# Kernel tuning notes

Measured on AMD Instinct MI355X. Metric: run time of the kernel, lower is better.

Reference implementation:

```python
import jax, jax.numpy as jnp
import numpy as np

WIN = 11  # hard-coded window size in the original module

def sinusoidal_pe(L, D):
    pos = jnp.arange(L, dtype=jnp.float32)[:, None]
    div = jnp.exp(jnp.arange(0, D, 2, dtype=jnp.float32) * (-np.log(10000.0) / D))
    pe = jnp.zeros((L, D), dtype=jnp.float32)
    pe = pe.at[:, 0::2].set(jnp.sin(pos * div))
    pe = pe.at[:, 1::2].set(jnp.cos(pos * div))
    return pe


def setup_inputs() -> dict:
    key = jax.random.key(0)
    ks = jax.random.split(key, 6)
    B, Lq, Ld, D, V = 16, 30, 1100, 768, 50000
    return {
        "q": jax.random.randint(ks[0], (B, Lq), 0, V),
        "d_pos": jax.random.randint(ks[1], (B, Ld), 0, V),
        "d_neg": jax.random.randint(ks[2], (B, Ld), 0, V),
        "q_mask": jnp.ones((B, Lq, 1), jnp.float32),
        "d_pos_mask": jnp.ones((B, Ld, 1), jnp.float32),
        "d_neg_mask": jnp.ones((B, Ld, 1), jnp.float32),
        "pe_flag": 1,
        "emb_table": jax.random.normal(ks[3], (V, D), jnp.float32) * 0.02,
        "W_lin": jax.random.normal(ks[4], (D, D), jnp.float32) * 0.02,
        "W_out": jax.random.normal(ks[5], (D, D), jnp.float32) * 0.02,
    }


def reference(q, d_pos, d_neg, q_mask, d_pos_mask, d_neg_mask, pe_flag, emb_table, W_lin, W_out):
    B, Lq = q.shape
    Ld = d_pos.shape[1]
    D = emb_table.shape[1]
    H = 12
    Dh = D // H
    W_num = Ld // WIN  # number of 11-token windows

    qe = emb_table[q] * q_mask              # [B,Lq,D]
    dp = emb_table[d_pos]                   # [B,Ld,D]
    dn = emb_table[d_neg]
    if pe_flag:
        pe = sinusoidal_pe(Ld, D)[None]     # [1,Ld,D]
        scale_emb = jnp.sqrt(jnp.float32(D))
        dp = dp * scale_emb + pe            # dropout p=0 -> identity
        dn = dn * scale_emb + pe
    dp = dp * d_pos_mask
    dn = dn * d_neg_mask

    dp = dp.reshape(B, W_num, WIN, D)       # [B,W,11,D]
    dn = dn.reshape(B, W_num, WIN, D)
    qx = jnp.broadcast_to(qe[:, None], (B, W_num, Lq, D))  # expand over windows

    # linear_trans (no bias): y = x @ W_lin.T
    queries = jnp.einsum('bwqd,ed->bwqe', qx, W_lin)
    dp = jnp.einsum('bwkd,ed->bwke', dp, W_lin)
    dn = jnp.einsum('bwkd,ed->bwke', dn, W_lin)

    # faithful replication of torch .view head-split: pure reshape, mixes seq+channel
    def split(x, L):
        return x.reshape(B, W_num, H, L, Dh)

    queries = split(queries, Lq) * (Dh ** -0.5)

    def attend(doc):
        d = split(doc, WIN)                                  # [B,W,H,11,Dh]
        logits = jnp.einsum('bwhqd,bwhkd->bwhqk', queries, d)
        weights = jax.nn.softmax(logits, axis=-1)            # dropout p=0
        ctx = jnp.einsum('bwhqk,bwhkd->bwhqd', weights, d)
        ctx = ctx.reshape(B, W_num, Lq, D)                   # faithful merge (.view)
        return jnp.einsum('bwqd,ed->bwqe', ctx, W_out)

    return attend(dp), attend(dn)
```

## Files before the change

kernel.cpp:

```cpp
#include <hip/hip_runtime.h>
#include <hip/hip_bf16.h>
#include <cstdint>
#include <cstddef>

#define B_    16
#define LQ    30
#define LD    1100
#define DIM   768
#define NH    12
#define DH_   64
#define WINSZ 11
#define WNUM  100
#define NSLOT 32

typedef __attribute__((ext_vector_type(8))) short short8;
typedef __attribute__((ext_vector_type(4))) float f32x4;

__device__ __forceinline__ void gload_lds16(const void* g, void* l) {
  __builtin_amdgcn_global_load_lds(
      (const __attribute__((address_space(1))) void*)g,
      (__attribute__((address_space(3))) void*)l, 16, 0, 0);
}

__global__ __launch_bounds__(256) void wconv_kernel(const float* __restrict__ wa,
    const float* __restrict__ wb, __hip_bfloat16* __restrict__ oa,
    __hip_bfloat16* __restrict__ ob) {
  int i = (blockIdx.x * 256 + threadIdx.x) * 4;
  if (i >= DIM * DIM) return;
  float4 va = *reinterpret_cast<const float4*>(wa + i);
  float4 vb = *reinterpret_cast<const float4*>(wb + i);
  union { __hip_bfloat16 h[4]; uint2 u; } pa, pb;
  pa.h[0] = __float2bfloat16(va.x); pa.h[1] = __float2bfloat16(va.y);
  pa.h[2] = __float2bfloat16(va.z); pa.h[3] = __float2bfloat16(va.w);
  pb.h[0] = __float2bfloat16(vb.x); pb.h[1] = __float2bfloat16(vb.y);
  pb.h[2] = __float2bfloat16(vb.z); pb.h[3] = __float2bfloat16(vb.w);
  *reinterpret_cast<uint2*>(oa + i) = pa.u;
  *reinterpret_cast<uint2*>(ob + i) = pb.u;
}

__global__ __launch_bounds__(256) void prep_q_kernel(const int* __restrict__ q,
    const float* __restrict__ qmask, const float* __restrict__ emb,
    __hip_bfloat16* __restrict__ Xq) {
  int idx = blockIdx.x * 256 + threadIdx.x;
  if (idx >= B_ * LQ * (DIM / 4)) return;
  int row = idx / (DIM / 4);
  int c4  = idx % (DIM / 4);
  float m = qmask[row] * 0.125f;
  float4 v = *reinterpret_cast<const float4*>(emb + (size_t)q[row] * DIM + c4 * 4);
  union { __hip_bfloat16 h[4]; uint2 u; } o;
  o.h[0] = __float2bfloat16(v.x * m); o.h[1] = __float2bfloat16(v.y * m);
  o.h[2] = __float2bfloat16(v.z * m); o.h[3] = __float2bfloat16(v.w * m);
  *reinterpret_cast<uint2*>(Xq + (size_t)row * DIM + c4 * 4) = o.u;
}

__global__ __launch_bounds__(256) void prep_d_kernel(const int* __restrict__ dpos,
    const int* __restrict__ dneg, const float* __restrict__ dpmask,
    const float* __restrict__ dnmask, const float* __restrict__ emb,
    const int* __restrict__ peflag, __hip_bfloat16* __restrict__ X,
    int s0, int rows) {
  int idx = blockIdx.x * 256 + threadIdx.x;
  if (idx >= rows * (DIM / 4)) return;
  int r  = idx / (DIM / 4);
  int c4 = idx % (DIM / 4);
  int s = s0 + r / LD;
  int t = r % LD;
  int doc = s >> 4, b = s & 15;
  const int*   di = doc ? dneg   : dpos;
  const float* dm = doc ? dnmask : dpmask;
  int grow = b * LD + t;
  float m = dm[grow];
  float4 v = *reinterpret_cast<const float4*>(emb + (size_t)di[grow] * DIM + c4 * 4);
  if (peflag[0]) {
    int i0 = c4 * 2;
    float d0 = expf(-0.023985261387f * (float)i0);
    float d1 = expf(-0.023985261387f * (float)(i0 + 1));
    float s0f, c0f, s1f, c1f;
    sincosf((float)t * d0, &s0f, &c0f);
    sincosf((float)t * d1, &s1f, &c1f);
    v.x = v.x * 27.712812921102035f + s0f;
    v.y = v.y * 27.712812921102035f + c0f;
    v.z = v.z * 27.712812921102035f + s1f;
    v.w = v.w * 27.712812921102035f + c1f;
  }
  union { __hip_bfloat16 h[4]; uint2 u; } o;
  o.h[0] = __float2bfloat16(v.x * m); o.h[1] = __float2bfloat16(v.y * m);
  o.h[2] = __float2bfloat16(v.z * m); o.h[3] = __float2bfloat16(v.w * m);
  *reinterpret_cast<uint2*>(X + (size_t)r * DIM + c4 * 4) = o.u;
}

template <bool OUT_BF16>
__global__ __launch_bounds__(512, 2) void gemm_mfma(const __hip_bfloat16* __restrict__ A,
    const __hip_bfloat16* __restrict__ Bt, void* __restrict__ Cv,
    int M, int N, int K, int tilesX) {
  extern __shared__ __hip_bfloat16 smem[];
  __hip_bfloat16* As = smem;
  __hip_bfloat16* Bs = smem + 4 * 8192;

  const int nwg  = gridDim.x;
  const int orig = blockIdx.x;
  const int q8 = nwg >> 3, r8 = nwg & 7;
  const int xcd = orig & 7, pos = orig >> 3;
  const int wgid = (xcd < r8 ? xcd * (q8 + 1) : r8 * (q8 + 1) + (xcd - r8) * q8) + pos;
  const int row0 = (wgid / tilesX) * 256;
  const int col0 = (wgid % tilesX) * 256;

  const int tid  = threadIdx.x;
  const int lane = tid & 63;
  const int wave = tid >> 6;
  const int wr = wave >> 2, wc = wave & 3;
  const int lo4 = lane & 15;

  const int csrc = (tid & 3) ^ ((tid >> 3) & 3);
  const __hip_bfloat16* gA = A  + (size_t)(row0 + (tid >> 2)) * K + csrc * 8;
  const __hip_bfloat16* gB = Bt + (size_t)(col0 + (tid >> 2)) * K + csrc * 8;

  const int coff = (((lane >> 4) ^ ((lo4 >> 1) & 3)) * 8);
  const int arow = (wr * 128 + lo4) * 32 + coff;
  const int brow = (wc * 64  + lo4) * 32 + coff;

  f32x4 acc[8][4] = {};

  auto STAGE = [&](int tt) {
    const int k0 = tt * 32;
    const int lo = (tt & 3) * 8192;
    gload_lds16(gA + k0,                   As + lo + tid * 8);
    gload_lds16(gA + (size_t)128 * K + k0, As + lo + 4096 + tid * 8);
    gload_lds16(gB + k0,                   Bs + lo + tid * 8);
    gload_lds16(gB + (size_t)128 * K + k0, Bs + lo + 4096 + tid * 8);
  };

#define MFMA4(MB)                                                       \
    _Pragma("unroll")                                                   \
    for (int n = 0; n < 4; ++n)                                         \
      acc[MB][n] = __builtin_amdgcn_mfma_f32_16x16x32_bf16(             \
          af0, bq[n], acc[MB][n], 0, 0, 0);                             \
    _Pragma("unroll")                                                   \
    for (int n = 0; n < 4; ++n)                                         \
      acc[MB + 1][n] = __builtin_amdgcn_mfma_f32_16x16x32_bf16(         \
          af1, bq[n], acc[MB + 1][n], 0, 0, 0);

#define STEP(tt, WAITN, DOSTAGE)                                        \
  {                                                                     \
    const int lo = ((tt) & 3) * 8192;                                   \
    const int so = (((tt) + 3) & 3) * 8192;                             \
    const int k0s = ((tt) + 3) * 32;                                    \
    const __hip_bfloat16* Ab = As + lo + arow;                          \
    const __hip_bfloat16* Bb = Bs + lo + brow;                          \
    short8 bq[4], af0, af1, af2, af3;                                   \
                                                 \
    asm volatile("s_waitcnt vmcnt(" WAITN ")" ::: "memory");            \
    __builtin_amdgcn_s_barrier();                                       \
    __builtin_amdgcn_sched_barrier(0);                                  \
    bq[0] = *reinterpret_cast<const short8*>(Bb);                       \
    bq[1] = *reinterpret_cast<const short8*>(Bb + 512);                 \
    bq[2] = *reinterpret_cast<const short8*>(Bb + 1024);                \
    bq[3] = *reinterpret_cast<const short8*>(Bb + 1536);                \
    af0 = *reinterpret_cast<const short8*>(Ab);                         \
    af1 = *reinterpret_cast<const short8*>(Ab + 512);                   \
    af2 = *reinterpret_cast<const short8*>(Ab + 1024);                  \
    af3 = *reinterpret_cast<const short8*>(Ab + 1536);                  \
    if (DOSTAGE) {                                                      \
      gload_lds16(gA + k0s,                   As + so + tid * 8);       \
      gload_lds16(gA + (size_t)128 * K + k0s, As + so + 4096 + tid * 8);\
    }                                                                   \
    asm volatile("s_waitcnt lgkmcnt(0)" ::: "memory");                  \
    __builtin_amdgcn_sched_barrier(0);                                  \
    __builtin_amdgcn_s_setprio(1);                                      \
    MFMA4(0)                                                            \
    { short8 t0 = af2, t1 = af3; af0 = t0; af1 = t1; }                  \
    MFMA4(2)                                                            \
    __builtin_amdgcn_s_setprio(0);                                      \
                                                 \
    __builtin_amdgcn_s_barrier();                                       \
    af0 = *reinterpret_cast<const short8*>(Ab + 2048);                  \
    af1 = *reinterpret_cast<const short8*>(Ab + 2560);                  \
    af2 = *reinterpret_cast<const short8*>(Ab + 3072);                  \
    af3 = *reinterpret_cast<const short8*>(Ab + 3584);                  \
    if (DOSTAGE) {                                                      \
      gload_lds16(gB + k0s,                   Bs + so + tid * 8);       \
      gload_lds16(gB + (size_t)128 * K + k0s, Bs + so + 4096 + tid * 8);\
    }                                                                   \
    asm volatile("s_waitcnt lgkmcnt(0)" ::: "memory");                  \
    __builtin_amdgcn_sched_barrier(0);                                  \
    __builtin_amdgcn_s_setprio(1);                                      \
    MFMA4(4)                                                            \
    { short8 t0 = af2, t1 = af3; af0 = t0; af1 = t1; }                  \
    MFMA4(6)                                                            \
    __builtin_amdgcn_s_setprio(0);                                      \
  }

  const int nt = K / 32;
  STAGE(0); STAGE(1); STAGE(2);
  for (int t = 0; t < nt - 3; ++t)
    STEP(t, "8", true)
  STEP(nt - 3, "8", false)
  STEP(nt - 2, "4", false)
  STEP(nt - 1, "0", false)
#undef STEP
#undef MFMA4

#pragma unroll
  for (int m = 0; m < 8; ++m) {
    int rb = row0 + wr * 128 + m * 16 + (lane >> 4) * 4;
#pragma unroll
    for (int n = 0; n < 4; ++n) {
      int c = col0 + wc * 64 + n * 16 + lo4;
      f32x4 v = acc[m][n];
#pragma unroll
      for (int j = 0; j < 4; ++j) {
        int r = rb + j;
        if (r < M) {
          if constexpr (OUT_BF16)
            ((__hip_bfloat16*)Cv)[(size_t)r * N + c] = __float2bfloat16(v[j]);
          else
            ((float*)Cv)[(size_t)r * N + c] = v[j];
        }
      }
    }
  }
}

__global__ __launch_bounds__(128) void attn_kernel(const float* __restrict__ Qs,
    const __hip_bfloat16* __restrict__ Y, __hip_bfloat16* __restrict__ ctx, int s0) {
  int blk = blockIdx.x;
  int h  = blk % NH;
  int w  = (blk / NH) % WNUM;
  int sl = blk / (NH * WNUM);
  int b  = (s0 + sl) & 15;

  __shared__ float Dl[WINSZ][DH_];

  const __hip_bfloat16* Yb = Y + ((size_t)(sl * LD + w * WINSZ)) * DIM + h * (WINSZ * DH_);
  const float* Qb = Qs + (size_t)b * (LQ * DIM) + h * (LQ * DH_);

  int tid = threadIdx.x;
  int qi = tid >> 2, part = tid & 3;

  if (tid < 88) {
    uint4 raw = *reinterpret_cast<const uint4*>(Yb + tid * 8);
    const __hip_bfloat16* hp = reinterpret_cast<const __hip_bfloat16*>(&raw);
    float* dst = &Dl[0][0] + tid * 8;
#pragma unroll
    for (int j = 0; j < 8; ++j) dst[j] = __bfloat162float(hp[j]);
  }

  float4 qreg[4];
#pragma unroll
  for (int j = 0; j < 4; ++j)
    qreg[j] = *reinterpret_cast<const float4*>(Qb + qi * DH_ + part * 16 + j * 4);
  __syncthreads();

  float dot[WINSZ];
#pragma unroll
  for (int k = 0; k < WINSZ; ++k) {
    const float4* dp = reinterpret_cast<const float4*>(&Dl[k][part * 16]);
    float s = 0.f;
#pragma unroll
    for (int j = 0; j < 4; ++j) {
      float4 dv = dp[j];
      s += qreg[j].x * dv.x + qreg[j].y * dv.y + qreg[j].z * dv.z + qreg[j].w * dv.w;
    }
    dot[k] = s;
  }
#pragma unroll
  for (int k = 0; k < WINSZ; ++k) {
    dot[k] += __shfl_xor(dot[k], 1);
    dot[k] += __shfl_xor(dot[k], 2);
  }
  float mx = -1e30f;
#pragma unroll
  for (int k = 0; k < WINSZ; ++k) mx = fmaxf(mx, dot[k]);
  float sum = 0.f;
#pragma unroll
  for (int k = 0; k < WINSZ; ++k) { dot[k] = expf(dot[k] - mx); sum += dot[k]; }
  float inv = 1.f / sum;

  float4 o[4] = {};
#pragma unroll
  for (int k = 0; k < WINSZ; ++k) {
    float pk = dot[k];
    const float4* dp = reinterpret_cast<const float4*>(&Dl[k][part * 16]);
#pragma unroll
    for (int j = 0; j < 4; ++j) {
      float4 dv = dp[j];
      o[j].x += pk * dv.x; o[j].y += pk * dv.y;
      o[j].z += pk * dv.z; o[j].w += pk * dv.w;
    }
  }
  union { __hip_bfloat16 hh[16]; uint4 v[2]; } pk;
#pragma unroll
  for (int j = 0; j < 4; ++j) {
    pk.hh[j * 4 + 0] = __float2bfloat16(o[j].x * inv);
    pk.hh[j * 4 + 1] = __float2bfloat16(o[j].y * inv);
    pk.hh[j * 4 + 2] = __float2bfloat16(o[j].z * inv);
    pk.hh[j * 4 + 3] = __float2bfloat16(o[j].w * inv);
  }
  __hip_bfloat16* op = ctx + (size_t)(sl * WNUM + w) * (LQ * DIM)
                     + h * (LQ * DH_) + qi * DH_ + part * 16;
  *reinterpret_cast<uint4*>(op)     = pk.v[0];
  *reinterpret_cast<uint4*>(op + 8) = pk.v[1];
}

extern "C" void kernel_launch(void* const* d_in, const int* in_sizes, int n_in,
                              void* d_out, int out_size, void* d_ws, size_t ws_size,
                              hipStream_t stream) {
  const int*   q      = (const int*)d_in[0];
  const int*   dpos   = (const int*)d_in[1];
  const int*   dneg   = (const int*)d_in[2];
  const float* qmask  = (const float*)d_in[3];
  const float* dpmask = (const float*)d_in[4];
  const float* dnmask = (const float*)d_in[5];
  const int*   peflag = (const int*)d_in[6];
  const float* emb    = (const float*)d_in[7];
  const float* Wlin   = (const float*)d_in[8];
  const float* Wout   = (const float*)d_in[9];
  float* out = (float*)d_out;

  (void)hipFuncSetAttribute(reinterpret_cast<const void*>(&gemm_mfma<false>),
                            hipFuncAttributeMaxDynamicSharedMemorySize, 131072);
  (void)hipFuncSetAttribute(reinterpret_cast<const void*>(&gemm_mfma<true>),
                            hipFuncAttributeMaxDynamicSharedMemorySize, 131072);

  char* ws = (char*)d_ws;
  size_t off = 0;
  auto alloc = [&](size_t bytes) -> char* {
    char* p = ws + off; off += (bytes + 255) & ~(size_t)255; return p;
  };
  __hip_bfloat16* Xq   = (__hip_bfloat16*)alloc((size_t)512 * DIM * 2);
  float*          Qsc  = (float*)         alloc((size_t)B_ * LQ * DIM * 4);
  __hip_bfloat16* Wl16 = (__hip_bfloat16*)alloc((size_t)DIM * DIM * 2);
  __hip_bfloat16* Wo16 = (__hip_bfloat16*)alloc((size_t)DIM * DIM * 2);

  int SC = NSLOT;
  while (SC > 1) {
    size_t need = off
        + ((size_t)SC * LD + 256) * DIM * 2 * 2
        + ((size_t)SC * WNUM * LQ + 256) * DIM * 2 + (1u << 20);
    if (need <= ws_size) break;
    SC >>= 1;
  }
  __hip_bfloat16* X   = (__hip_bfloat16*)alloc(((size_t)SC * LD + 256) * DIM * 2);
  __hip_bfloat16* Y   = (__hip_bfloat16*)alloc(((size_t)SC * LD + 256) * DIM * 2);
  __hip_bfloat16* ctx = (__hip_bfloat16*)alloc(((size_t)SC * WNUM * LQ + 256) * DIM * 2);

  wconv_kernel<<<(DIM * DIM / 4 + 255) / 256, 256, 0, stream>>>(Wlin, Wout, Wl16, Wo16);
  prep_q_kernel<<<(B_ * LQ * (DIM / 4) + 255) / 256, 256, 0, stream>>>(q, qmask, emb, Xq);
  {
    int tilesX = DIM / 256, tilesY = (B_ * LQ + 255) / 256;
    gemm_mfma<false><<<tilesX * tilesY, 512, 131072, stream>>>(
        Xq, Wl16, Qsc, B_ * LQ, DIM, DIM, tilesX);
  }

  for (int s0 = 0; s0 < NSLOT; s0 += SC) {
    const int rowsX = SC * LD;
    const int rowsC = SC * WNUM * LQ;
    prep_d_kernel<<<(rowsX * (DIM / 4) + 255) / 256, 256, 0, stream>>>(
        dpos, dneg, dpmask, dnmask, emb, peflag, X, s0, rowsX);
    {
      int tilesX = DIM / 256, tilesY = (rowsX + 255) / 256;
      gemm_mfma<true><<<tilesX * tilesY, 512, 131072, stream>>>(
          X, Wl16, Y, rowsX, DIM, DIM, tilesX);
    }
    attn_kernel<<<SC * WNUM * NH, 120, 0, stream>>>(Qsc, Y, ctx, s0);
    {
      int tilesX = DIM / 256, tilesY = (rowsC + 255) / 256;
      gemm_mfma<false><<<tilesX * tilesY, 512, 131072, stream>>>(
          ctx, Wo16, out + (size_t)s0 * WNUM * LQ * DIM, rowsC, DIM, DIM, tilesX);
    }
  }
}
```

Baseline: 399.7 us.

## Fold query projection GEMM into document GEMM launch and vectorize epilogue stores

The separate query-projection GEMM launch is removed, and its tiles are appended to the first document-projection GEMM grid, with a per-block selector choosing the A matrix and output. The MFMA operand order is swapped so each lane holds four consecutive output columns. That lets the epilogue write vector stores (f32x4 or 4 packed bf16) instead of scalar strided stores. This saves one kernel launch and makes output writes coalesced and wider, at the cost of per-block branching and a heterogeneous grid.

```diff
diff --git a/kernel.cpp b/kernel.cpp
--- a/kernel.cpp
+++ b/kernel.cpp
@@ -91,7 +91,8 @@
 template <bool OUT_BF16>
 __global__ __launch_bounds__(512, 2) void gemm_mfma(const __hip_bfloat16* __restrict__ A,
     const __hip_bfloat16* __restrict__ Bt, void* __restrict__ Cv,
-    int M, int N, int K, int tilesX) {
+    int M, int N, int K, int tilesX, int tiles1,
+    const __hip_bfloat16* __restrict__ A2, float* __restrict__ C2, int M2) {
   extern __shared__ __hip_bfloat16 smem[];
   __hip_bfloat16* As = smem;
   __hip_bfloat16* Bs = smem + 4 * 8192;
@@ -101,20 +102,26 @@
   const int q8 = nwg >> 3, r8 = nwg & 7;
   const int xcd = orig & 7, pos = orig >> 3;
   const int wgid = (xcd < r8 ? xcd * (q8 + 1) : r8 * (q8 + 1) + (xcd - r8) * q8) + pos;
-  const int row0 = (wgid / tilesX) * 256;
-  const int col0 = (wgid % tilesX) * 256;
+
+  const bool is2 = (wgid >= tiles1);
+  const int  w2  = is2 ? (wgid - tiles1) : wgid;
+  const int row0 = (w2 / tilesX) * 256;
+  const int col0 = (w2 % tilesX) * 256;
+  const __hip_bfloat16* Ap = is2 ? A2 : A;
+  const int Mloc = is2 ? M2 : M;
 
   const int tid  = threadIdx.x;
   const int lane = tid & 63;
   const int wave = tid >> 6;
   const int wr = wave >> 2, wc = wave & 3;
   const int lo4 = lane & 15;
+  const int hi4 = lane >> 4;
 
   const int csrc = (tid & 3) ^ ((tid >> 3) & 3);
-  const __hip_bfloat16* gA = A  + (size_t)(row0 + (tid >> 2)) * K + csrc * 8;
+  const __hip_bfloat16* gA = Ap + (size_t)(row0 + (tid >> 2)) * K + csrc * 8;
   const __hip_bfloat16* gB = Bt + (size_t)(col0 + (tid >> 2)) * K + csrc * 8;
 
-  const int coff = (((lane >> 4) ^ ((lo4 >> 1) & 3)) * 8);
+  const int coff = ((hi4 ^ ((lo4 >> 1) & 3)) * 8);
   const int arow = (wr * 128 + lo4) * 32 + coff;
   const int brow = (wc * 64  + lo4) * 32 + coff;
 
@@ -133,11 +140,11 @@
     _Pragma("unroll")                                                   \
     for (int n = 0; n < 4; ++n)                                         \
       acc[MB][n] = __builtin_amdgcn_mfma_f32_16x16x32_bf16(             \
-          af0, bq[n], acc[MB][n], 0, 0, 0);                             \
+          bq[n], af0, acc[MB][n], 0, 0, 0);                             \
     _Pragma("unroll")                                                   \
     for (int n = 0; n < 4; ++n)                                         \
       acc[MB + 1][n] = __builtin_amdgcn_mfma_f32_16x16x32_bf16(         \
-          af1, bq[n], acc[MB + 1][n], 0, 0, 0);
+          bq[n], af1, acc[MB + 1][n], 0, 0, 0);
 
 #define STEP(tt, WAITN, DOSTAGE)                                        \
   {                                                                     \
@@ -201,19 +208,21 @@
 
 #pragma unroll
   for (int m = 0; m < 8; ++m) {
-    int rb = row0 + wr * 128 + m * 16 + (lane >> 4) * 4;
-#pragma unroll
-    for (int n = 0; n < 4; ++n) {
-      int c = col0 + wc * 64 + n * 16 + lo4;
-      f32x4 v = acc[m][n];
-#pragma unroll
-      for (int j = 0; j < 4; ++j) {
-        int r = rb + j;
-        if (r < M) {
-          if constexpr (OUT_BF16)
-            ((__hip_bfloat16*)Cv)[(size_t)r * N + c] = __float2bfloat16(v[j]);
-          else
-            ((float*)Cv)[(size_t)r * N + c] = v[j];
+    const int r = row0 + wr * 128 + m * 16 + lo4;
+    if (r < Mloc) {
+#pragma unroll
+      for (int n = 0; n < 4; ++n) {
+        const int cb = col0 + wc * 64 + n * 16 + hi4 * 4;
+        f32x4 v = acc[m][n];
+        if (is2) {
+          *reinterpret_cast<f32x4*>(C2 + (size_t)r * N + cb) = v;
+        } else if constexpr (OUT_BF16) {
+          union { __hip_bfloat16 h[4]; uint2 u; } p;
+          p.h[0] = __float2bfloat16(v[0]); p.h[1] = __float2bfloat16(v[1]);
+          p.h[2] = __float2bfloat16(v[2]); p.h[3] = __float2bfloat16(v[3]);
+          *reinterpret_cast<uint2*>((__hip_bfloat16*)Cv + (size_t)r * N + cb) = p.u;
+        } else {
+          *reinterpret_cast<f32x4*>((float*)Cv + (size_t)r * N + cb) = v;
         }
       }
     }
@@ -345,11 +354,9 @@
 
   wconv_kernel<<<(DIM * DIM / 4 + 255) / 256, 256, 0, stream>>>(Wlin, Wout, Wl16, Wo16);
   prep_q_kernel<<<(B_ * LQ * (DIM / 4) + 255) / 256, 256, 0, stream>>>(q, qmask, emb, Xq);
-  {
-    int tilesX = DIM / 256, tilesY = (B_ * LQ + 255) / 256;
-    gemm_mfma<false><<<tilesX * tilesY, 512, 131072, stream>>>(
-        Xq, Wl16, Qsc, B_ * LQ, DIM, DIM, tilesX);
-  }
+
+  const int tilesX = DIM / 256;
+  const int qTiles = tilesX * ((B_ * LQ + 255) / 256);
 
   for (int s0 = 0; s0 < NSLOT; s0 += SC) {
     const int rowsX = SC * LD;
@@ -357,15 +364,17 @@
     prep_d_kernel<<<(rowsX * (DIM / 4) + 255) / 256, 256, 0, stream>>>(
         dpos, dneg, dpmask, dnmask, emb, peflag, X, s0, rowsX);
     {
-      int tilesX = DIM / 256, tilesY = (rowsX + 255) / 256;
-      gemm_mfma<true><<<tilesX * tilesY, 512, 131072, stream>>>(
-          X, Wl16, Y, rowsX, DIM, DIM, tilesX);
+      int tiles1 = tilesX * ((rowsX + 255) / 256);
+      int t2 = (s0 == 0) ? qTiles : 0;
+      gemm_mfma<true><<<tiles1 + t2, 512, 131072, stream>>>(
+          X, Wl16, Y, rowsX, DIM, DIM, tilesX, tiles1, Xq, Qsc, B_ * LQ);
     }
     attn_kernel<<<SC * WNUM * NH, 120, 0, stream>>>(Qsc, Y, ctx, s0);
     {
-      int tilesX = DIM / 256, tilesY = (rowsC + 255) / 256;
-      gemm_mfma<false><<<tilesX * tilesY, 512, 131072, stream>>>(
-          ctx, Wo16, out + (size_t)s0 * WNUM * LQ * DIM, rowsC, DIM, DIM, tilesX);
-    }
-  }
-}
+      int tiles1 = tilesX * ((rowsC + 255) / 256);
+      gemm_mfma<false><<<tiles1, 512, 131072, stream>>>(
+          ctx, Wo16, out + (size_t)s0 * WNUM * LQ * DIM, rowsC, DIM, DIM,
+          tilesX, tiles1, nullptr, nullptr, 0);
+    }
+  }
+}
```

Result: faster. 385.4 us (-3.6%).
